# Kernel optimization log

Hardware: AMD Instinct MI355X
Metric: run time of the kernel (lower is better)

Reference implementation:

```python
import jax, jax.numpy as jnp
import numpy as np

UNITS = 256
IN_DIM = 256


def setup_inputs() -> dict:
    key = jax.random.key(0)
    ks = jax.random.split(key, 8)
    B, T, D, U = 128, 512, IN_DIM, UNITS
    scale = 1.0 / np.sqrt(D + U)
    x = jax.random.normal(ks[0], (B, T, D), dtype=jnp.float32)
    h0 = jnp.zeros((B, U), dtype=jnp.float32)
    Wr = jax.random.normal(ks[1], (D + U, U), dtype=jnp.float32) * scale
    br = jnp.zeros((U,), dtype=jnp.float32)
    Wz = jax.random.normal(ks[2], (D + U, U), dtype=jnp.float32) * scale
    bz = jnp.zeros((U,), dtype=jnp.float32)
    Wc = jax.random.normal(ks[3], (D + U, U), dtype=jnp.float32) * scale
    bc = jnp.zeros((U,), dtype=jnp.float32)
    return {"x": x, "h0": h0, "Wr": Wr, "br": br, "Wz": Wz, "bz": bz, "Wc": Wc, "bc": bc}


def reference(x, h0, Wr, br, Wz, bz, Wc, bc):
    # x: [B, T, D]; h0: [B, U]. Runs the custom GRU cell over T steps.
    def step(h, xt):
        xh = jnp.concatenate([xt, h], axis=-1)            # [B, D+U]
        r = jax.nn.sigmoid(xh @ Wr + br)                  # reset gate
        z = jax.nn.sigmoid(xh @ Wz + bz)                  # update gate
        xc = jnp.concatenate([xt, r * h], axis=-1)
        c = jnp.tanh(xc @ Wc + bc)                        # candidate
        h_new = (1.0 - z) * h + z * c
        return h_new, h_new

    xs = jnp.swapaxes(x, 0, 1)                            # [T, B, D]
    _, ys = jax.lax.scan(step, h0, xs)                    # ys: [T, B, U]
    return jnp.swapaxes(ys, 0, 1)                         # [B, T, U]
```

## Files before the change

kernel.cpp:

```cpp
#include <hip/hip_runtime.h>
#include <hip/hip_fp16.h>

typedef _Float16 h2 __attribute__((ext_vector_type(2)));
typedef _Float16 h8 __attribute__((ext_vector_type(8)));
typedef float f4 __attribute__((ext_vector_type(4)));
typedef float f4v __attribute__((ext_vector_type(4)));

#define NB 128
#define NT 512
#define ND 256
#define NU 256

__device__ __forceinline__ float fdot2f(h2 a, h2 b, float c) {
#if __has_builtin(__builtin_amdgcn_fdot2)
  return __builtin_amdgcn_fdot2(a, b, c, false);
#else
  return c + (float)a[0] * (float)b[0] + (float)a[1] * (float)b[1];
#endif
}

__device__ __forceinline__ h2 pick2(h8 v, int j) {
  h2 r;
  r[0] = v[2 * j];
  r[1] = v[2 * j + 1];
  return r;
}

__device__ __forceinline__ float fast_rcp(float x) {
  return __builtin_amdgcn_rcpf(x);
}

__global__ void k_prep(const float* __restrict__ Wr, const float* __restrict__ Wz,
                       const float* __restrict__ Wc, _Float16* __restrict__ WT,
                       _Float16* __restrict__ WhT) {
  int idx = blockIdx.x * 256 + threadIdx.x;
  int g = idx >> 16;
  int r = idx & 65535;
  int u = r >> 8;
  int k = r & 255;
  const float* W = (g == 0) ? Wr : ((g == 1) ? Wz : Wc);
  WT[idx]  = (_Float16)W[k * NU + u];
  WhT[idx] = (_Float16)W[(ND + k) * NU + u];
}

#define BM 128
#define BN 128
#define BK 32
#define LDT 40

__global__ __launch_bounds__(256) void k_gemm(const float* __restrict__ x,
                                              const _Float16* __restrict__ WT,
                                              const float* __restrict__ br,
                                              const float* __restrict__ bz,
                                              const float* __restrict__ bc,
                                              _Float16* __restrict__ gx) {
  __shared__ alignas(16) _Float16 Al[BM * LDT];
  __shared__ alignas(16) _Float16 Bl[BN * LDT];
  const int n0 = blockIdx.x * BN;
  const int m0 = blockIdx.y * BM;
  const int tid = threadIdx.x;
  const int lane = tid & 63;
  const int wid = tid >> 6;
  const int mb = (wid >> 1) * 64;
  const int nb = (wid & 1) * 64;

  f4 acc[4][4] = {};

  for (int k0 = 0; k0 < 256; k0 += BK) {
    __syncthreads();
    {
      int row = tid >> 1;
      int seg = (tid & 1) * 16;
      const float* src = x + (size_t)(m0 + row) * ND + k0 + seg;
      f4v f0 = *(const f4v*)(src);
      f4v f1 = *(const f4v*)(src + 4);
      f4v f2 = *(const f4v*)(src + 8);
      f4v f3 = *(const f4v*)(src + 12);
      h8 w0, w1;
#pragma unroll
      for (int j = 0; j < 4; j++) {
        w0[j] = (_Float16)f0[j];
        w0[4 + j] = (_Float16)f1[j];
        w1[j] = (_Float16)f2[j];
        w1[4 + j] = (_Float16)f3[j];
      }
      *(h8*)&Al[row * LDT + seg] = w0;
      *(h8*)&Al[row * LDT + seg + 8] = w1;
    }
    {
      int row = tid >> 1;
      int seg = (tid & 1) * 16;
      const _Float16* src = WT + (size_t)(n0 + row) * 256 + k0 + seg;
      h8 w0 = *(const h8*)(src);
      h8 w1 = *(const h8*)(src + 8);
      *(h8*)&Bl[row * LDT + seg] = w0;
      *(h8*)&Bl[row * LDT + seg + 8] = w1;
    }
    __syncthreads();
    h8 af[4], bf[4];
#pragma unroll
    for (int mt = 0; mt < 4; mt++)
      af[mt] = *(const h8*)&Al[(mb + mt * 16 + (lane & 15)) * LDT + (lane >> 4) * 8];
#pragma unroll
    for (int nt = 0; nt < 4; nt++)
      bf[nt] = *(const h8*)&Bl[(nb + nt * 16 + (lane & 15)) * LDT + (lane >> 4) * 8];
#pragma unroll
    for (int mt = 0; mt < 4; mt++)
#pragma unroll
      for (int nt = 0; nt < 4; nt++)
        acc[mt][nt] = __builtin_amdgcn_mfma_f32_16x16x32_f16(af[mt], bf[nt], acc[mt][nt], 0, 0, 0);
  }

  const float* bias = (n0 < 256) ? br : ((n0 < 512) ? bz : bc);
#pragma unroll
  for (int nt = 0; nt < 4; nt++) {
    int col = nb + nt * 16 + (lane & 15);
    float bv = bias[(n0 + col) & 255];
#pragma unroll
    for (int mt = 0; mt < 4; mt++) {
#pragma unroll
      for (int r = 0; r < 4; r++) {
        int row = mb + mt * 16 + (lane >> 4) * 4 + r;
        float v = acc[mt][nt][r] + bv;
        gx[(size_t)(m0 + row) * 768 + n0 + col] = (_Float16)v;
      }
    }
  }
}

__global__ __launch_bounds__(512, 2) void k_gru(const float* __restrict__ h0,
                                                const _Float16* __restrict__ WhT,
                                                const _Float16* __restrict__ gx,
                                                float* __restrict__ out) {
  __shared__ alignas(16) _Float16 h16[NU];
  __shared__ alignas(16) float h32[NU];
  __shared__ alignas(16) _Float16 rh16[NU];
  __shared__ alignas(16) float zls[NU];
  __shared__ alignas(16) float cpart[512];

  const int b = blockIdx.x;
  const int tid = threadIdx.x;
  const int u = tid & 255;
  const int half = tid >> 8;

  h2 wrz[128];
#pragma unroll
  for (int i = 0; i < 32; i++) {
    h8 w = *(const h8*)(WhT + ((size_t)(half * 256 + u)) * 256 + i * 8);
#pragma unroll
    for (int j = 0; j < 4; j++) wrz[i * 4 + j] = pick2(w, j);
  }
  h2 wc[64];
#pragma unroll
  for (int i = 0; i < 16; i++) {
    h8 w = *(const h8*)(WhT + ((size_t)(2 * 256 + u)) * 256 + half * 128 + i * 8);
#pragma unroll
    for (int j = 0; j < 4; j++) wc[i * 4 + j] = pick2(w, j);
  }

  if (tid < NU) {
    float h = h0[(size_t)b * NU + tid];
    h32[tid] = h;
    h16[tid] = (_Float16)h;
  }
  __syncthreads();

  const _Float16* gb = gx + (size_t)b * NT * 768;
  float ga = (float)gb[half * 256 + u];
  float gc = (float)gb[512 + u];

  for (int t = 0; t < NT; t++) {
    int tn = (t + 1 < NT) ? t + 1 : t;
    _Float16 nga = gb[(size_t)tn * 768 + half * 256 + u];
    _Float16 ngc = gb[(size_t)tn * 768 + 512 + u];

    float a0 = 0.f, a1 = 0.f, a2 = 0.f, a3 = 0.f;
#pragma unroll
    for (int kk = 0; kk < 32; kk++) {
      h8 hv = *(const h8*)&h16[kk * 8];
      a0 = fdot2f(pick2(hv, 0), wrz[kk * 4 + 0], a0);
      a1 = fdot2f(pick2(hv, 1), wrz[kk * 4 + 1], a1);
      a2 = fdot2f(pick2(hv, 2), wrz[kk * 4 + 2], a2);
      a3 = fdot2f(pick2(hv, 3), wrz[kk * 4 + 3], a3);
    }
    float pre = (a0 + a1) + (a2 + a3) + ga;
    float e = __expf(-pre);
    float s = fast_rcp(1.f + e);
    if (half == 0) {
      rh16[u] = (_Float16)(s * h32[u]);
    } else {
      zls[u] = s;
    }
    __syncthreads();

    float c0 = 0.f, c1 = 0.f;
#pragma unroll
    for (int kk = 0; kk < 16; kk++) {
      h8 hv = *(const h8*)&rh16[half * 128 + kk * 8];
      c0 = fdot2f(pick2(hv, 0), wc[kk * 4 + 0], c0);
      c1 = fdot2f(pick2(hv, 1), wc[kk * 4 + 1], c1);
      c0 = fdot2f(pick2(hv, 2), wc[kk * 4 + 2], c0);
      c1 = fdot2f(pick2(hv, 3), wc[kk * 4 + 3], c1);
    }
    cpart[tid] = c0 + c1;
    __syncthreads();

    if (half == 0) {
      float pc = cpart[u] + cpart[256 + u] + gc;
      pc = fminf(fmaxf(pc, -15.f), 15.f);
      float e2 = __expf(2.f * pc);
      float c = (e2 - 1.f) * fast_rcp(e2 + 1.f);
      float z = zls[u];
      float h = h32[u];
      float hn = h + z * (c - h);
      h32[u] = hn;
      h16[u] = (_Float16)hn;
      out[((size_t)b * NT + t) * NU + u] = hn;
    }
    ga = (float)nga;
    gc = (float)ngc;
    __syncthreads();
  }
}

extern "C" void kernel_launch(void* const* d_in, const int* in_sizes, int n_in,
                              void* d_out, int out_size, void* d_ws, size_t ws_size,
                              hipStream_t stream) {
  (void)in_sizes; (void)n_in; (void)out_size; (void)ws_size;
  const float* x  = (const float*)d_in[0];
  const float* h0 = (const float*)d_in[1];
  const float* Wr = (const float*)d_in[2];
  const float* br = (const float*)d_in[3];
  const float* Wz = (const float*)d_in[4];
  const float* bz = (const float*)d_in[5];
  const float* Wc = (const float*)d_in[6];
  const float* bc = (const float*)d_in[7];
  float* out = (float*)d_out;

  _Float16* gx  = (_Float16*)d_ws;
  _Float16* WT  = gx + (size_t)NB * NT * 768;
  _Float16* WhT = WT + 3 * 256 * 256;

  k_prep<<<768, 256, 0, stream>>>(Wr, Wz, Wc, WT, WhT);
  k_gemm<<<dim3(6, 512), 256, 0, stream>>>(x, WT, br, bz, bc, gx);
  k_gru<<<NB, 512, 0, stream>>>(h0, WhT, gx, out);
}
```

Before: 870.9 us.

## Split GRU recurrence into three 256-thread gate groups per block

The recurrent kernel moves from 512 threads (two halves sharing r/z rows and splitting the candidate dot product with a partial-sum reduction) to 768 threads, one group each for r, z and candidate. The candidate group runs the full 256-wide dot product by itself, which removes the cpart shared buffer and its extra reduction pass, and it keeps h in a register. Each thread now holds 128 packed weight registers instead of 192. In exchange, the candidate group sits idle during the r/z phase and the r/z groups sit idle during the candidate phase, so the serial critical path per step may get longer.

```diff
diff --git a/kernel.cpp b/kernel.cpp
--- a/kernel.cpp
+++ b/kernel.cpp
@@ -128,97 +128,101 @@
   }
 }
 
-__global__ __launch_bounds__(512, 2) void k_gru(const float* __restrict__ h0,
-                                                const _Float16* __restrict__ WhT,
-                                                const _Float16* __restrict__ gx,
-                                                float* __restrict__ out) {
+__global__ __launch_bounds__(768) void k_gru(const float* __restrict__ h0,
+                                             const _Float16* __restrict__ WhT,
+                                             const _Float16* __restrict__ gx,
+                                             float* __restrict__ out) {
   __shared__ alignas(16) _Float16 h16[NU];
   __shared__ alignas(16) float h32[NU];
   __shared__ alignas(16) _Float16 rh16[NU];
   __shared__ alignas(16) float zls[NU];
-  __shared__ alignas(16) float cpart[512];
 
   const int b = blockIdx.x;
   const int tid = threadIdx.x;
   const int u = tid & 255;
-  const int half = tid >> 8;
-
-  h2 wrz[128];
-#pragma unroll
-  for (int i = 0; i < 32; i++) {
-    h8 w = *(const h8*)(WhT + ((size_t)(half * 256 + u)) * 256 + i * 8);
-#pragma unroll
-    for (int j = 0; j < 4; j++) wrz[i * 4 + j] = pick2(w, j);
-  }
-  h2 wc[64];
-#pragma unroll
-  for (int i = 0; i < 16; i++) {
-    h8 w = *(const h8*)(WhT + ((size_t)(2 * 256 + u)) * 256 + half * 128 + i * 8);
-#pragma unroll
-    for (int j = 0; j < 4; j++) wc[i * 4 + j] = pick2(w, j);
-  }
-
-  if (tid < NU) {
-    float h = h0[(size_t)b * NU + tid];
-    h32[tid] = h;
-    h16[tid] = (_Float16)h;
+  const int g = tid >> 8;
+
+  h2 w[128];
+  {
+    const _Float16* wp = WhT + ((size_t)(g * 256 + u)) * 256;
+#pragma unroll
+    for (int i = 0; i < 32; i++) {
+      h8 v = *(const h8*)(wp + i * 8);
+#pragma unroll
+      for (int j = 0; j < 4; j++) w[i * 4 + j] = pick2(v, j);
+    }
+  }
+
+  float hreg = 0.f;
+  if (g == 2) {
+    hreg = h0[(size_t)b * NU + u];
+    h32[u] = hreg;
+    h16[u] = (_Float16)hreg;
   }
   __syncthreads();
 
   const _Float16* gb = gx + (size_t)b * NT * 768;
-  float ga = (float)gb[half * 256 + u];
-  float gc = (float)gb[512 + u];
+  float ga = (float)gb[g * 256 + u];
 
   for (int t = 0; t < NT; t++) {
     int tn = (t + 1 < NT) ? t + 1 : t;
-    _Float16 nga = gb[(size_t)tn * 768 + half * 256 + u];
-    _Float16 ngc = gb[(size_t)tn * 768 + 512 + u];
-
-    float a0 = 0.f, a1 = 0.f, a2 = 0.f, a3 = 0.f;
-#pragma unroll
-    for (int kk = 0; kk < 32; kk++) {
-      h8 hv = *(const h8*)&h16[kk * 8];
-      a0 = fdot2f(pick2(hv, 0), wrz[kk * 4 + 0], a0);
-      a1 = fdot2f(pick2(hv, 1), wrz[kk * 4 + 1], a1);
-      a2 = fdot2f(pick2(hv, 2), wrz[kk * 4 + 2], a2);
-      a3 = fdot2f(pick2(hv, 3), wrz[kk * 4 + 3], a3);
-    }
-    float pre = (a0 + a1) + (a2 + a3) + ga;
-    float e = __expf(-pre);
-    float s = fast_rcp(1.f + e);
-    if (half == 0) {
-      rh16[u] = (_Float16)(s * h32[u]);
-    } else {
-      zls[u] = s;
-    }
-    __syncthreads();
-
-    float c0 = 0.f, c1 = 0.f;
-#pragma unroll
-    for (int kk = 0; kk < 16; kk++) {
-      h8 hv = *(const h8*)&rh16[half * 128 + kk * 8];
-      c0 = fdot2f(pick2(hv, 0), wc[kk * 4 + 0], c0);
-      c1 = fdot2f(pick2(hv, 1), wc[kk * 4 + 1], c1);
-      c0 = fdot2f(pick2(hv, 2), wc[kk * 4 + 2], c0);
-      c1 = fdot2f(pick2(hv, 3), wc[kk * 4 + 3], c1);
-    }
-    cpart[tid] = c0 + c1;
-    __syncthreads();
-
-    if (half == 0) {
-      float pc = cpart[u] + cpart[256 + u] + gc;
+    _Float16 nga = gb[(size_t)tn * 768 + g * 256 + u];
+
+    if (g < 2) {
+      float a0 = 0.f, a1 = 0.f, a2 = 0.f, a3 = 0.f;
+      float a4 = 0.f, a5 = 0.f, a6 = 0.f, a7 = 0.f;
+#pragma unroll
+      for (int i = 0; i < 16; i++) {
+        h8 hv0 = *(const h8*)&h16[i * 16];
+        h8 hv1 = *(const h8*)&h16[i * 16 + 8];
+        a0 = fdot2f(pick2(hv0, 0), w[i * 8 + 0], a0);
+        a1 = fdot2f(pick2(hv0, 1), w[i * 8 + 1], a1);
+        a2 = fdot2f(pick2(hv0, 2), w[i * 8 + 2], a2);
+        a3 = fdot2f(pick2(hv0, 3), w[i * 8 + 3], a3);
+        a4 = fdot2f(pick2(hv1, 0), w[i * 8 + 4], a4);
+        a5 = fdot2f(pick2(hv1, 1), w[i * 8 + 5], a5);
+        a6 = fdot2f(pick2(hv1, 2), w[i * 8 + 6], a6);
+        a7 = fdot2f(pick2(hv1, 3), w[i * 8 + 7], a7);
+      }
+      float pre = ((a0 + a1) + (a2 + a3)) + ((a4 + a5) + (a6 + a7)) + ga;
+      float e = __expf(-pre);
+      float s = fast_rcp(1.f + e);
+      if (g == 0) {
+        rh16[u] = (_Float16)(s * h32[u]);
+      } else {
+        zls[u] = s;
+      }
+    }
+    __syncthreads();
+
+    if (g == 2) {
+      float a0 = 0.f, a1 = 0.f, a2 = 0.f, a3 = 0.f;
+      float a4 = 0.f, a5 = 0.f, a6 = 0.f, a7 = 0.f;
+#pragma unroll
+      for (int i = 0; i < 16; i++) {
+        h8 hv0 = *(const h8*)&rh16[i * 16];
+        h8 hv1 = *(const h8*)&rh16[i * 16 + 8];
+        a0 = fdot2f(pick2(hv0, 0), w[i * 8 + 0], a0);
+        a1 = fdot2f(pick2(hv0, 1), w[i * 8 + 1], a1);
+        a2 = fdot2f(pick2(hv0, 2), w[i * 8 + 2], a2);
+        a3 = fdot2f(pick2(hv0, 3), w[i * 8 + 3], a3);
+        a4 = fdot2f(pick2(hv1, 0), w[i * 8 + 4], a4);
+        a5 = fdot2f(pick2(hv1, 1), w[i * 8 + 5], a5);
+        a6 = fdot2f(pick2(hv1, 2), w[i * 8 + 6], a6);
+        a7 = fdot2f(pick2(hv1, 3), w[i * 8 + 7], a7);
+      }
+      float pc = ((a0 + a1) + (a2 + a3)) + ((a4 + a5) + (a6 + a7)) + ga;
       pc = fminf(fmaxf(pc, -15.f), 15.f);
       float e2 = __expf(2.f * pc);
       float c = (e2 - 1.f) * fast_rcp(e2 + 1.f);
       float z = zls[u];
-      float h = h32[u];
-      float hn = h + z * (c - h);
+      float hn = hreg + z * (c - hreg);
+      hreg = hn;
+      h16[u] = (_Float16)hn;
       h32[u] = hn;
-      h16[u] = (_Float16)hn;
       out[((size_t)b * NT + t) * NU + u] = hn;
     }
     ga = (float)nga;
-    gc = (float)ngc;
     __syncthreads();
   }
 }
@@ -243,5 +247,5 @@
 
   k_prep<<<768, 256, 0, stream>>>(Wr, Wz, Wc, WT, WhT);
   k_gemm<<<dim3(6, 512), 256, 0, stream>>>(x, WT, br, bz, bc, gx);
-  k_gru<<<NB, 512, 0, stream>>>(h0, WhT, gx, out);
-}
+  k_gru<<<NB, 768, 0, stream>>>(h0, WhT, gx, out);
+}
```

Measured after the change: 959.5 us. +10.2%, slower.
